# Kernel tuning notes

Measured on AMD Instinct MI355X. Metric: run time of the kernel, lower is better.

## Reference

```python
import jax, jax.numpy as jnp
import numpy as np

B, S, H, DH = 2, 4096, 8, 64
D = H * DH  # 512

def setup_inputs() -> dict:
    key = jax.random.key(0)
    ks = jax.random.split(key, 9)
    sc = 1.0 / np.sqrt(D)
    return {
        "hidden_states": jax.random.normal(ks[0], (B, S, D), jnp.float32),
        "Wq": jax.random.normal(ks[1], (D, D), jnp.float32) * sc,
        "bq": jax.random.normal(ks[2], (D,), jnp.float32) * 0.02,
        "Wk": jax.random.normal(ks[3], (D, D), jnp.float32) * sc,
        "bk": jax.random.normal(ks[4], (D,), jnp.float32) * 0.02,
        "Wv": jax.random.normal(ks[5], (D, D), jnp.float32) * sc,
        "bv": jax.random.normal(ks[6], (D,), jnp.float32) * 0.02,
        "Wo": jax.random.normal(ks[7], (D, D), jnp.float32) * sc,
        "bo": jax.random.normal(ks[8], (D,), jnp.float32) * 0.02,
    }

def _split_heads(t):
    # (B, S, H*DH) -> (B, H, S, DH)
    b = t.shape[0]
    return t.reshape(b, S, H, DH).transpose(0, 2, 1, 3)

def reference(hidden_states, Wq, bq, Wk, bk, Wv, bv, Wo, bo):
    q = _split_heads(hidden_states @ Wq + bq)
    k = _split_heads(hidden_states @ Wk + bk)
    v = _split_heads(hidden_states @ Wv + bv)
    scale = 1.0 / jnp.sqrt(jnp.asarray(DH, q.dtype))
    energy = jnp.einsum('bhqd,bhkd->bhqk', q, k) * scale
    weights = jax.nn.softmax(energy, axis=-1)  # full O(S^2) matrix, as in source
    attended = jnp.einsum('bhqv,bhvd->bhqd', weights, v)
    merged = attended.transpose(0, 2, 1, 3).reshape(hidden_states.shape[0], S, D)
    return merged @ Wo + bo
```

## Files before the change

kernel.cpp:

```cpp
#include <hip/hip_runtime.h>
#include <cstdint>

typedef __bf16 bf16;
typedef __bf16 bf16x8 __attribute__((ext_vector_type(8)));
typedef float floatx4 __attribute__((ext_vector_type(4)));

#define MFMA32(a, b, c) __builtin_amdgcn_mfma_f32_16x16x32_bf16((a), (b), (c), 0, 0, 0)

__device__ inline bf16x8 cvt8(const float* p) {
    float4 u = *(const float4*)p;
    float4 v = *(const float4*)(p + 4);
    bf16x8 r;
    r[0] = (bf16)u.x; r[1] = (bf16)u.y; r[2] = (bf16)u.z; r[3] = (bf16)u.w;
    r[4] = (bf16)v.x; r[5] = (bf16)v.y; r[6] = (bf16)v.z; r[7] = (bf16)v.w;
    return r;
}

__global__ __launch_bounds__(256) void k_transpose(
    const float* __restrict__ w0, const float* __restrict__ w1,
    const float* __restrict__ w2, const float* __restrict__ w3,
    bf16* __restrict__ o0, bf16* __restrict__ o1,
    bf16* __restrict__ o2, bf16* __restrict__ o3)
{
    __shared__ float t[32][33];
    const float* in;
    bf16* out;
    switch (blockIdx.z) {
        case 0: in = w0; out = o0; break;
        case 1: in = w1; out = o1; break;
        case 2: in = w2; out = o2; break;
        default: in = w3; out = o3; break;
    }
    const int tx = threadIdx.x & 31;
    const int ty = threadIdx.x >> 5;
    const int r0 = blockIdx.y * 32;
    const int c0 = blockIdx.x * 32;
    #pragma unroll
    for (int i = 0; i < 32; i += 8)
        t[ty + i][tx] = in[(size_t)(r0 + ty + i) * 512 + c0 + tx];
    __syncthreads();
    #pragma unroll
    for (int i = 0; i < 32; i += 8)
        out[(size_t)(c0 + ty + i) * 512 + r0 + tx] = (bf16)t[tx][ty + i];
}

__global__ __launch_bounds__(256) void k_cvtx(
    const float* __restrict__ X, bf16* __restrict__ Xb)
{
    const size_t idx = ((size_t)blockIdx.x * 256 + threadIdx.x) * 8;
    *(bf16x8*)(Xb + idx) = cvt8(X + idx);
}

__global__ __launch_bounds__(256) void k_qkv(
    const bf16* __restrict__ Xb, const bf16* __restrict__ Wcat,
    const float* __restrict__ bq, const float* __restrict__ bk, const float* __restrict__ bv,
    bf16* __restrict__ Qs, bf16* __restrict__ Ks, bf16* __restrict__ Vt)
{
    __shared__ __align__(16) unsigned char smem[36864];
    uint4* Al = (uint4*)smem;
    uint4* Bl = (uint4*)(smem + 16384);

    const int tid  = threadIdx.x;
    const int w    = tid >> 6;
    const int lane = tid & 63;
    const int col  = lane & 15;
    const int quad = lane >> 4;
    const int m0 = blockIdx.x * 128;
    const int n0 = blockIdx.y * 128;

    const bf16* gA0 = Xb   + (size_t)(m0 + (tid >> 2)) * 512 + (tid & 3) * 8;
    const bf16* gA1 = gA0 + 64 * 512;
    const bf16* gB0 = Wcat + (size_t)(n0 + (tid >> 2)) * 512 + (tid & 3) * 8;
    const bf16* gB1 = gB0 + 64 * 512;

    const floatx4 zf = {0.f, 0.f, 0.f, 0.f};
    floatx4 acc[4][4];
    #pragma unroll
    for (int a = 0; a < 4; ++a)
        #pragma unroll
        for (int b = 0; b < 4; ++b) acc[a][b] = zf;

    Al[tid]       = *(const uint4*)gA0;
    Al[tid + 256] = *(const uint4*)gA1;
    Bl[tid]       = *(const uint4*)gB0;
    Bl[tid + 256] = *(const uint4*)gB1;
    __syncthreads();

    const int mb = (w & 1) * 64;
    const int nb = (w >> 1) * 64;

    int buf = 0;
    for (int kk = 0; kk < 16; ++kk) {
        const int kn = ((kk + 1) & 15) * 32;
        const uint4 pa0 = *(const uint4*)(gA0 + kn);
        const uint4 pa1 = *(const uint4*)(gA1 + kn);
        const uint4 pb0 = *(const uint4*)(gB0 + kn);
        const uint4 pb1 = *(const uint4*)(gB1 + kn);

        const uint4* A4 = Al + buf * 512;
        const uint4* B4 = Bl + buf * 512;
        bf16x8 af[4], bfr[4];
        #pragma unroll
        for (int t = 0; t < 4; ++t) {
            union { uint4 u; bf16x8 v; } ca, cb;
            ca.u = A4[(mb + 16 * t + col) * 4 + quad];
            cb.u = B4[(nb + 16 * t + col) * 4 + quad];
            af[t] = ca.v;
            bfr[t] = cb.v;
        }
        #pragma unroll
        for (int tm = 0; tm < 4; ++tm)
            #pragma unroll
            for (int tn = 0; tn < 4; ++tn)
                acc[tm][tn] = MFMA32(af[tm], bfr[tn], acc[tm][tn]);

        const int nbuf = buf ^ 1;
        Al[nbuf * 512 + tid]       = pa0;
        Al[nbuf * 512 + tid + 256] = pa1;
        Bl[nbuf * 512 + tid]       = pb0;
        Bl[nbuf * 512 + tid + 256] = pb1;
        __syncthreads();
        buf = nbuf;
    }

    bf16* ep = (bf16*)smem + (size_t)w * 64 * 72;

    const int which = blockIdx.y >> 2;
    const int nbase = (blockIdx.y & 3) * 128 + nb;
    const int h  = nbase >> 6;
    const int mw = m0 + mb;
    const int b  = mw >> 12;
    const int s0 = mw & 4095;
    const float qsc = 0.125f * 1.44269504088896f;

    if (which == 2) {
        #pragma unroll
        for (int tn = 0; tn < 4; ++tn) {
            const int d = 16 * tn + col;
            const float bb = bv[nbase + d];
            #pragma unroll
            for (int tm = 0; tm < 4; ++tm) {
                union { bf16 e[4]; uint2 u; } pk;
                #pragma unroll
                for (int r = 0; r < 4; ++r) pk.e[r] = (bf16)(acc[tm][tn][r] + bb);
                *(uint2*)(ep + d * 72 + 16 * tm + 4 * quad) = pk.u;
            }
        }
    } else {
        const float* bias = (which == 0) ? bq : bk;
        const float sc = (which == 0) ? qsc : 1.0f;
        #pragma unroll
        for (int tn = 0; tn < 4; ++tn) {
            const int d = 16 * tn + col;
            const float bb = bias[nbase + d];
            #pragma unroll
            for (int tm = 0; tm < 4; ++tm)
                #pragma unroll
                for (int r = 0; r < 4; ++r)
                    ep[(16 * tm + 4 * quad + r) * 72 + d] = (bf16)((acc[tm][tn][r] + bb) * sc);
        }
    }

    asm volatile("" ::: "memory");

    const int rl = lane >> 3;
    const int ch = lane & 7;
    bf16* gbase;
    size_t rowstride;
    if (which == 2) {
        gbase = Vt + (((size_t)b * 8 + h) * 64) * 4096 + s0;
        rowstride = 4096;
    } else {
        bf16* P = (which == 0) ? Qs : Ks;
        gbase = P + (((size_t)b * 8 + h) * 4096 + s0) * 64;
        rowstride = 64;
    }
    #pragma unroll
    for (int it = 0; it < 8; ++it) {
        const int row = it * 8 + rl;
        const uint4 v = *(const uint4*)(ep + row * 72 + ch * 8);
        *(uint4*)(gbase + (size_t)row * rowstride + ch * 8) = v;
    }
}

__global__ __launch_bounds__(256, 2) void k_attn(
    const bf16* __restrict__ Qs, const bf16* __restrict__ Ks, const bf16* __restrict__ Vt,
    bf16* __restrict__ att)
{
    __shared__ uint4 Klds[2][256];
    __shared__ uint4 Vlds[2][256];
    __shared__ uint32_t Pt_all[4 * 32 * 17];

    const int tid  = threadIdx.x;
    const int w    = tid >> 6;
    const int lane = tid & 63;
    const int col  = lane & 15;
    const int quad = lane >> 4;
    const int i    = blockIdx.x;
    const int bh   = ((i & 7) << 1) | ((i >> 3) & 1);
    const int q0   = (i >> 4) * 128 + w * 32;

    const bf16* Qb = Qs + (size_t)bh * 262144;
    const bf16* Kb = Ks + (size_t)bh * 262144;
    const bf16* Vb = Vt + (size_t)bh * 262144;
    uint32_t* Pt = Pt_all + w * 32 * 17;

    const int rK  = tid >> 3;
    const int lcK = (tid & 7) ^ (rK & 7);
    const bf16* gK = Kb + (size_t)rK * 64 + lcK * 8;
    const int pV  = tid >> 3;
    const int ccV = (tid & 7) ^ (pV & 7);
    const int dV  = 2 * pV + (ccV >> 2);
    const int cV  = ccV & 3;
    const bf16* gV = Vb + (size_t)dV * 4096 + cV * 8;

    bf16x8 aq[2][2];
    #pragma unroll
    for (int s = 0; s < 2; ++s)
        #pragma unroll
        for (int c = 0; c < 2; ++c)
            aq[s][c] = *(const bf16x8*)(Qb + (size_t)(q0 + 16 * s + col) * 64 + 32 * c + quad * 8);

    const floatx4 zf = {0.f, 0.f, 0.f, 0.f};
    floatx4 o[2][4];
    float l[2][4];
    #pragma unroll
    for (int s = 0; s < 2; ++s) {
        #pragma unroll
        for (int t = 0; t < 4; ++t) o[s][t] = zf;
        #pragma unroll
        for (int r = 0; r < 4; ++r) l[s][r] = 0.f;
    }

    const uint32_t sel = (col & 1) ? 0x07060302u : 0x05040100u;

    Klds[0][tid] = *(const uint4*)gK;
    Vlds[0][tid] = *(const uint4*)gV;
    __syncthreads();

    int buf = 0;
    for (int kt = 0; kt < 4096; kt += 32) {
        const int kn = (kt + 32) & 4095;
        const uint4 kreg = *(const uint4*)(gK + (size_t)kn * 64);
        const uint4 vreg = *(const uint4*)(gV + kn);

        const uint4* Kl = Klds[buf];
        const uint4* Vl = Vlds[buf];
        bf16x8 kf[2][2], vf[4];
        #pragma unroll
        for (int t = 0; t < 2; ++t)
            #pragma unroll
            for (int h = 0; h < 2; ++h) {
                union { uint4 u; bf16x8 v; } cv;
                cv.u = Kl[(16 * t + col) * 8 + ((quad + 4 * h) ^ (col & 7))];
                kf[t][h] = cv.v;
            }
        #pragma unroll
        for (int t = 0; t < 4; ++t) {
            union { uint4 u; bf16x8 v; } cv;
            cv.u = Vl[(8 * t + (col >> 1)) * 8 + ((((col & 1) * 4) + quad) ^ ((col >> 1) & 7))];
            vf[t] = cv.v;
        }

        #pragma unroll
        for (int s = 0; s < 2; ++s) {
            #pragma unroll
            for (int t = 0; t < 2; ++t) {
                floatx4 sc = MFMA32(aq[s][1], kf[t][1], MFMA32(aq[s][0], kf[t][0], zf));
                float p0 = __builtin_amdgcn_exp2f(sc[0]);
                float p1 = __builtin_amdgcn_exp2f(sc[1]);
                float p2 = __builtin_amdgcn_exp2f(sc[2]);
                float p3 = __builtin_amdgcn_exp2f(sc[3]);
                l[s][0] += p0; l[s][1] += p1; l[s][2] += p2; l[s][3] += p3;
                union { bf16 e[4]; uint32_t u[2]; } pk;
                pk.e[0] = (bf16)p0; pk.e[1] = (bf16)p1;
                pk.e[2] = (bf16)p2; pk.e[3] = (bf16)p3;
                uint32_t* dst = Pt + (16 * t + col) * 17 + 8 * s + 2 * quad;
                dst[0] = pk.u[0];
                dst[1] = pk.u[1];
            }
        }
        #pragma unroll
        for (int s = 0; s < 2; ++s) {
            uint32_t wd[8];
            #pragma unroll
            for (int j = 0; j < 8; ++j)
                wd[j] = Pt[(quad * 8 + j) * 17 + 8 * s + (col >> 1)];
            union { uint32_t u[4]; bf16x8 v; } ap;
            #pragma unroll
            for (int ii = 0; ii < 4; ++ii)
                ap.u[ii] = __builtin_amdgcn_perm(wd[2 * ii + 1], wd[2 * ii], sel);
            #pragma unroll
            for (int t = 0; t < 4; ++t)
                o[s][t] = MFMA32(ap.v, vf[t], o[s][t]);
        }

        Klds[buf ^ 1][tid] = kreg;
        Vlds[buf ^ 1][tid] = vreg;
        __syncthreads();
        buf ^= 1;
    }

    #pragma unroll
    for (int s = 0; s < 2; ++s)
        #pragma unroll
        for (int r = 0; r < 4; ++r) {
            float v = l[s][r];
            v += __shfl_xor(v, 1, 64);
            v += __shfl_xor(v, 2, 64);
            v += __shfl_xor(v, 4, 64);
            v += __shfl_xor(v, 8, 64);
            l[s][r] = 1.0f / v;
        }

    const int b = bh >> 3;
    const int h = bh & 7;
    #pragma unroll
    for (int s = 0; s < 2; ++s)
        #pragma unroll
        for (int t = 0; t < 4; ++t)
            #pragma unroll
            for (int r = 0; r < 4; ++r) {
                const size_t row = (size_t)b * 4096 + q0 + 16 * s + 4 * quad + r;
                att[row * 512 + h * 64 + 16 * t + col] = (bf16)(o[s][t][r] * l[s][r]);
            }
}

__global__ __launch_bounds__(256) void k_oproj(
    const bf16* __restrict__ att, const bf16* __restrict__ Wto,
    const float* __restrict__ bo, float* __restrict__ out)
{
    __shared__ uint4 Al[2][512];
    __shared__ uint4 Bl[2][512];

    const int tid  = threadIdx.x;
    const int w    = tid >> 6;
    const int lane = tid & 63;
    const int col  = lane & 15;
    const int quad = lane >> 4;
    const int m0 = blockIdx.x * 128;
    const int n0 = blockIdx.y * 128;

    const bf16* gA0 = att + (size_t)(m0 + (tid >> 2)) * 512 + (tid & 3) * 8;
    const bf16* gA1 = gA0 + 64 * 512;
    const bf16* gB0 = Wto + (size_t)(n0 + (tid >> 2)) * 512 + (tid & 3) * 8;
    const bf16* gB1 = gB0 + 64 * 512;

    const floatx4 zf = {0.f, 0.f, 0.f, 0.f};
    floatx4 acc[4][4];
    #pragma unroll
    for (int a = 0; a < 4; ++a)
        #pragma unroll
        for (int b = 0; b < 4; ++b) acc[a][b] = zf;

    Al[0][tid]       = *(const uint4*)gA0;
    Al[0][tid + 256] = *(const uint4*)gA1;
    Bl[0][tid]       = *(const uint4*)gB0;
    Bl[0][tid + 256] = *(const uint4*)gB1;
    __syncthreads();

    const int mb = (w & 1) * 64;
    const int nb = (w >> 1) * 64;

    int buf = 0;
    for (int kk = 0; kk < 16; ++kk) {
        const int kn = ((kk + 1) & 15) * 32;
        const uint4 pa0 = *(const uint4*)(gA0 + kn);
        const uint4 pa1 = *(const uint4*)(gA1 + kn);
        const uint4 pb0 = *(const uint4*)(gB0 + kn);
        const uint4 pb1 = *(const uint4*)(gB1 + kn);

        const uint4* A4 = Al[buf];
        const uint4* B4 = Bl[buf];
        bf16x8 af[4], bfr[4];
        #pragma unroll
        for (int t = 0; t < 4; ++t) {
            union { uint4 u; bf16x8 v; } ca, cb;
            ca.u = A4[(mb + 16 * t + col) * 4 + quad];
            cb.u = B4[(nb + 16 * t + col) * 4 + quad];
            af[t] = ca.v;
            bfr[t] = cb.v;
        }
        #pragma unroll
        for (int tm = 0; tm < 4; ++tm)
            #pragma unroll
            for (int tn = 0; tn < 4; ++tn)
                acc[tm][tn] = MFMA32(af[tm], bfr[tn], acc[tm][tn]);

        Al[buf ^ 1][tid]       = pa0;
        Al[buf ^ 1][tid + 256] = pa1;
        Bl[buf ^ 1][tid]       = pb0;
        Bl[buf ^ 1][tid + 256] = pb1;
        __syncthreads();
        buf ^= 1;
    }

    #pragma unroll
    for (int tn = 0; tn < 4; ++tn) {
        const int n = n0 + nb + 16 * tn + col;
        const float bb = bo[n];
        #pragma unroll
        for (int tm = 0; tm < 4; ++tm)
            #pragma unroll
            for (int r = 0; r < 4; ++r) {
                const int m = m0 + mb + 16 * tm + quad * 4 + r;
                out[(size_t)m * 512 + n] = acc[tm][tn][r] + bb;
            }
    }
}

extern "C" void kernel_launch(void* const* d_in, const int* in_sizes, int n_in,
                              void* d_out, int out_size, void* d_ws, size_t ws_size,
                              hipStream_t stream)
{
    const float* X  = (const float*)d_in[0];
    const float* Wq = (const float*)d_in[1];
    const float* bq = (const float*)d_in[2];
    const float* Wk = (const float*)d_in[3];
    const float* bk = (const float*)d_in[4];
    const float* Wv = (const float*)d_in[5];
    const float* bv = (const float*)d_in[6];
    const float* Wo = (const float*)d_in[7];
    const float* bo = (const float*)d_in[8];

    bf16* Wtq = (bf16*)d_ws;
    bf16* Wtk = Wtq + 512 * 512;
    bf16* Wtv = Wtk + 512 * 512;
    bf16* Wto = Wtv + 512 * 512;
    bf16* Qs  = Wto + 512 * 512;
    bf16* Ks  = Qs + (size_t)16 * 4096 * 64;
    bf16* Vt  = Ks + (size_t)16 * 4096 * 64;
    bf16* att = Vt + (size_t)16 * 4096 * 64;

    bf16* Xb  = (bf16*)d_out;

    k_transpose<<<dim3(16, 16, 4), 256, 0, stream>>>(Wq, Wk, Wv, Wo, Wtq, Wtk, Wtv, Wto);
    k_cvtx<<<2048, 256, 0, stream>>>(X, Xb);
    k_qkv<<<dim3(64, 12), 256, 0, stream>>>(Xb, Wtq, bq, bk, bv, Qs, Ks, Vt);
    k_attn<<<512, 256, 0, stream>>>(Qs, Ks, Vt, att);
    k_oproj<<<dim3(64, 4), 256, 0, stream>>>(att, Wto, bo, (float*)d_out);
}
```

Baseline: 219.9 us.

## Compute transposed scores so P feeds PV MFMA from registers, drop LDS round-trip

```diff
diff --git a/kernel.cpp b/kernel.cpp
--- a/kernel.cpp
+++ b/kernel.cpp
@@ -2,10 +2,12 @@
 #include <cstdint>
 
 typedef __bf16 bf16;
+typedef __bf16 bf16x4 __attribute__((ext_vector_type(4)));
 typedef __bf16 bf16x8 __attribute__((ext_vector_type(8)));
 typedef float floatx4 __attribute__((ext_vector_type(4)));
 
 #define MFMA32(a, b, c) __builtin_amdgcn_mfma_f32_16x16x32_bf16((a), (b), (c), 0, 0, 0)
+#define MFMA16(a, b, c) __builtin_amdgcn_mfma_f32_16x16x16bf16_1k((a), (b), (c), 0, 0, 0)
 
 __device__ inline bf16x8 cvt8(const float* p) {
     float4 u = *(const float4*)p;
@@ -189,7 +191,6 @@
 {
     __shared__ uint4 Klds[2][256];
     __shared__ uint4 Vlds[2][256];
-    __shared__ uint32_t Pt_all[4 * 32 * 17];
 
     const int tid  = threadIdx.x;
     const int w    = tid >> 6;
@@ -203,7 +204,6 @@
     const bf16* Qb = Qs + (size_t)bh * 262144;
     const bf16* Kb = Ks + (size_t)bh * 262144;
     const bf16* Vb = Vt + (size_t)bh * 262144;
-    uint32_t* Pt = Pt_all + w * 32 * 17;
 
     const int rK  = tid >> 3;
     const int lcK = (tid & 7) ^ (rK & 7);
@@ -223,16 +223,13 @@
 
     const floatx4 zf = {0.f, 0.f, 0.f, 0.f};
     floatx4 o[2][4];
-    float l[2][4];
-    #pragma unroll
-    for (int s = 0; s < 2; ++s) {
-        #pragma unroll
-        for (int t = 0; t < 4; ++t) o[s][t] = zf;
-        #pragma unroll
-        for (int r = 0; r < 4; ++r) l[s][r] = 0.f;
-    }
-
-    const uint32_t sel = (col & 1) ? 0x07060302u : 0x05040100u;
+    float lsum[2] = {0.f, 0.f};
+    #pragma unroll
+    for (int s = 0; s < 2; ++s)
+        #pragma unroll
+        for (int dt = 0; dt < 4; ++dt) o[s][dt] = zf;
+
+    const int c1 = col & 1, ch = col >> 1, qh = quad >> 1, ql = quad & 1;
 
     Klds[0][tid] = *(const uint4*)gK;
     Vlds[0][tid] = *(const uint4*)gV;
@@ -245,54 +242,49 @@
         const uint4 vreg = *(const uint4*)(gV + kn);
 
         const uint4* Kl = Klds[buf];
-        const uint4* Vl = Vlds[buf];
-        bf16x8 kf[2][2], vf[4];
+        const uint2* Vl = (const uint2*)Vlds[buf];
+
+        bf16x8 kf[2][2];
         #pragma unroll
         for (int t = 0; t < 2; ++t)
             #pragma unroll
-            for (int h = 0; h < 2; ++h) {
+            for (int c = 0; c < 2; ++c) {
                 union { uint4 u; bf16x8 v; } cv;
-                cv.u = Kl[(16 * t + col) * 8 + ((quad + 4 * h) ^ (col & 7))];
-                kf[t][h] = cv.v;
-            }
-        #pragma unroll
-        for (int t = 0; t < 4; ++t) {
-            union { uint4 u; bf16x8 v; } cv;
-            cv.u = Vl[(8 * t + (col >> 1)) * 8 + ((((col & 1) * 4) + quad) ^ ((col >> 1) & 7))];
-            vf[t] = cv.v;
-        }
+                cv.u = Kl[(16 * t + col) * 8 + ((quad + 4 * c) ^ (col & 7))];
+                kf[t][c] = cv.v;
+            }
+        bf16x4 vfrag[4][2];
+        #pragma unroll
+        for (int dt = 0; dt < 4; ++dt)
+            #pragma unroll
+            for (int t = 0; t < 2; ++t) {
+                const int slot = (dt * 8 + ch) * 8 + ((c1 * 4 + 2 * t + qh) ^ ch);
+                union { uint2 u; bf16x4 v; } cv;
+                cv.u = Vl[slot * 2 + ql];
+                vfrag[dt][t] = cv.v;
+            }
 
         #pragma unroll
         for (int s = 0; s < 2; ++s) {
+            bf16x4 pw[2];
             #pragma unroll
             for (int t = 0; t < 2; ++t) {
-                floatx4 sc = MFMA32(aq[s][1], kf[t][1], MFMA32(aq[s][0], kf[t][0], zf));
-                float p0 = __builtin_amdgcn_exp2f(sc[0]);
-                float p1 = __builtin_amdgcn_exp2f(sc[1]);
-                float p2 = __builtin_amdgcn_exp2f(sc[2]);
-                float p3 = __builtin_amdgcn_exp2f(sc[3]);
-                l[s][0] += p0; l[s][1] += p1; l[s][2] += p2; l[s][3] += p3;
-                union { bf16 e[4]; uint32_t u[2]; } pk;
+                floatx4 sc = MFMA32(kf[t][1], aq[s][1], MFMA32(kf[t][0], aq[s][0], zf));
+                const float p0 = __builtin_amdgcn_exp2f(sc[0]);
+                const float p1 = __builtin_amdgcn_exp2f(sc[1]);
+                const float p2 = __builtin_amdgcn_exp2f(sc[2]);
+                const float p3 = __builtin_amdgcn_exp2f(sc[3]);
+                lsum[s] += (p0 + p1) + (p2 + p3);
+                union { bf16 e[4]; bf16x4 v; } pk;
                 pk.e[0] = (bf16)p0; pk.e[1] = (bf16)p1;
                 pk.e[2] = (bf16)p2; pk.e[3] = (bf16)p3;
-                uint32_t* dst = Pt + (16 * t + col) * 17 + 8 * s + 2 * quad;
-                dst[0] = pk.u[0];
-                dst[1] = pk.u[1];
-            }
-        }
-        #pragma unroll
-        for (int s = 0; s < 2; ++s) {
-            uint32_t wd[8];
-            #pragma unroll
-            for (int j = 0; j < 8; ++j)
-                wd[j] = Pt[(quad * 8 + j) * 17 + 8 * s + (col >> 1)];
-            union { uint32_t u[4]; bf16x8 v; } ap;
-            #pragma unroll
-            for (int ii = 0; ii < 4; ++ii)
-                ap.u[ii] = __builtin_amdgcn_perm(wd[2 * ii + 1], wd[2 * ii], sel);
-            #pragma unroll
-            for (int t = 0; t < 4; ++t)
-                o[s][t] = MFMA32(ap.v, vf[t], o[s][t]);
+                pw[t] = pk.v;
+            }
+            #pragma unroll
+            for (int dt = 0; dt < 4; ++dt) {
+                o[s][dt] = MFMA16(vfrag[dt][0], pw[0], o[s][dt]);
+                o[s][dt] = MFMA16(vfrag[dt][1], pw[1], o[s][dt]);
+            }
         }
 
         Klds[buf ^ 1][tid] = kreg;
@@ -301,29 +293,27 @@
         buf ^= 1;
     }
 
-    #pragma unroll
-    for (int s = 0; s < 2; ++s)
-        #pragma unroll
-        for (int r = 0; r < 4; ++r) {
-            float v = l[s][r];
-            v += __shfl_xor(v, 1, 64);
-            v += __shfl_xor(v, 2, 64);
-            v += __shfl_xor(v, 4, 64);
-            v += __shfl_xor(v, 8, 64);
-            l[s][r] = 1.0f / v;
-        }
+    float inv[2];
+    #pragma unroll
+    for (int s = 0; s < 2; ++s) {
+        float v = lsum[s];
+        v += __shfl_xor(v, 16, 64);
+        v += __shfl_xor(v, 32, 64);
+        inv[s] = 1.0f / v;
+    }
 
     const int b = bh >> 3;
     const int h = bh & 7;
     #pragma unroll
     for (int s = 0; s < 2; ++s)
         #pragma unroll
-        for (int t = 0; t < 4; ++t)
-            #pragma unroll
-            for (int r = 0; r < 4; ++r) {
-                const size_t row = (size_t)b * 4096 + q0 + 16 * s + 4 * quad + r;
-                att[row * 512 + h * 64 + 16 * t + col] = (bf16)(o[s][t][r] * l[s][r]);
-            }
+        for (int dt = 0; dt < 4; ++dt) {
+            union { bf16 e[4]; uint2 u; } pk;
+            #pragma unroll
+            for (int r = 0; r < 4; ++r) pk.e[r] = (bf16)(o[s][dt][r] * inv[s]);
+            const size_t row = (size_t)b * 4096 + q0 + 16 * s + col;
+            *(uint2*)(att + row * 512 + h * 64 + 16 * dt + 4 * quad) = pk.u;
+        }
 }
 
 __global__ __launch_bounds__(256) void k_oproj(
```

Result: faster. 205.1 us (-6.7%).
